# Kernel optimization log

Hardware: AMD Instinct MI355X
Metric: run time of the kernel (lower is better)

Reference implementation:

```python
import jax, jax.numpy as jnp
import numpy as np

B, N, D = 2, 2048, 1024
H = 16
HD = D // H  # head_dim = 64
EPS = 1e-5


def _layernorm(x, gamma, beta):
    mu = jnp.mean(x, axis=-1, keepdims=True)
    var = jnp.var(x, axis=-1, keepdims=True)
    return (x - mu) * jax.lax.rsqrt(var + EPS) * gamma + beta


def setup_inputs() -> dict:
    key = jax.random.key(0)
    ks = jax.random.split(key, 13)
    s = 1.0 / np.sqrt(D)
    return {
        "query": jax.random.normal(ks[0], (B, N, D), dtype=jnp.float32),
        "Wq": jax.random.uniform(ks[1], (D, D), jnp.float32, -s, s),
        "bq": jax.random.uniform(ks[2], (D,), jnp.float32, -s, s),
        "Wk": jax.random.uniform(ks[3], (D, D), jnp.float32, -s, s),
        "bk": jax.random.uniform(ks[4], (D,), jnp.float32, -s, s),
        "Wv": jax.random.uniform(ks[5], (D, D), jnp.float32, -s, s),
        "bv": jax.random.uniform(ks[6], (D,), jnp.float32, -s, s),
        "Wp": jax.random.uniform(ks[7], (D, D), jnp.float32, -s, s),
        "bp": jax.random.uniform(ks[8], (D,), jnp.float32, -s, s),
        "q_gamma": jnp.ones((HD,), jnp.float32),
        "q_beta": jnp.zeros((HD,), jnp.float32),
        "k_gamma": jnp.ones((HD,), jnp.float32),
        "k_beta": jnp.zeros((HD,), jnp.float32),
    }


def reference(query, Wq, bq, Wk, bk, Wv, bv, Wp, bp, q_gamma, q_beta, k_gamma, k_beta):
    # Linear projections (torch Linear: x @ W.T + b)
    def split_heads(x):  # [B,N,D] -> [B,H,N,HD]
        return x.reshape(B, N, H, HD).transpose(0, 2, 1, 3)

    Q = split_heads(query @ Wq.T + bq)
    K = split_heads(query @ Wk.T + bk)
    V = split_heads(query @ Wv.T + bv)

    # per-head QK LayerNorm
    Q = _layernorm(Q, q_gamma, q_beta)
    K = _layernorm(K, k_gamma, k_beta)

    scale = 1.0 / np.sqrt(HD)
    attn = jax.nn.softmax(jnp.einsum('bhqd,bhkd->bhqk', Q, K) * scale, axis=-1)
    # dropout_prob = 0.0 -> identity
    out = jnp.einsum('bhqk,bhkd->bqhd', attn, V).reshape(B, N, D)
    return out @ Wp.T + bp
```

## Files before the change

### kernel.cpp

```cpp
#include <hip/hip_runtime.h>
#include <math.h>

#define Bb 2
#define Nn 2048
#define Dd 1024
#define Hh 16
#define HD 64

typedef __attribute__((ext_vector_type(8))) short short8;
typedef __attribute__((ext_vector_type(4))) short short4v;
typedef __attribute__((ext_vector_type(4))) float floatx4;

__device__ __forceinline__ short f2bf(float x) {
    unsigned u = __float_as_uint(x);
    u += 0x7fffu + ((u >> 16) & 1u);
    return (short)(u >> 16);
}

#if defined(__has_builtin)
#  if __has_builtin(__builtin_amdgcn_mfma_f32_16x16x16bf16_1k)
#    define MFMA16(a, b, c) __builtin_amdgcn_mfma_f32_16x16x16bf16_1k(a, b, c, 0, 0, 0)
#  endif
#endif
#ifndef MFMA16
static __device__ __forceinline__ floatx4 mfma16_asm(short4v a, short4v b, floatx4 c) {
    asm volatile("v_mfma_f32_16x16x16_bf16 %0, %1, %2, %0" : "+v"(c) : "v"(a), "v"(b));
    return c;
}
#  define MFMA16(a, b, c) mfma16_asm(a, b, c)
#endif

__device__ __forceinline__ void gload16(const void* g, void* l) {
    __builtin_amdgcn_global_load_lds(
        (const __attribute__((address_space(1))) unsigned int*)g,
        (__attribute__((address_space(3))) unsigned int*)l,
        16, 0, 0);
}

#define QSCALE 0.18033688011112042f

__global__ __launch_bounds__(256) void cast_all(
    const float* __restrict__ x,
    const float* __restrict__ Wq, const float* __restrict__ Wk,
    const float* __restrict__ Wv, const float* __restrict__ Wp,
    short* __restrict__ xh, short* __restrict__ Wqh, short* __restrict__ Wkh,
    short* __restrict__ Wvh, short* __restrict__ Wph)
{
    const float* src; short* dst; int n4;
    switch (blockIdx.y) {
        case 0:  src = x;  dst = xh;  n4 = (Bb * Nn * Dd) / 4; break;
        case 1:  src = Wq; dst = Wqh; n4 = (Dd * Dd) / 4; break;
        case 2:  src = Wk; dst = Wkh; n4 = (Dd * Dd) / 4; break;
        case 3:  src = Wv; dst = Wvh; n4 = (Dd * Dd) / 4; break;
        default: src = Wp; dst = Wph; n4 = (Dd * Dd) / 4; break;
    }
    const int i = blockIdx.x * 256 + threadIdx.x;
    if (i >= n4) return;
    float4 v = ((const float4*)src)[i];
    short4v o;
    o.x = f2bf(v.x); o.y = f2bf(v.y); o.z = f2bf(v.z); o.w = f2bf(v.w);
    ((short4v*)dst)[i] = o;
}

__global__ __launch_bounds__(256) void qkv_ln_gemm(
    const short* __restrict__ xh,
    const short* __restrict__ Wqh, const short* __restrict__ Wkh,
    const short* __restrict__ Wvh,
    const float* __restrict__ bq, const float* __restrict__ bk,
    const float* __restrict__ bv,
    const float* __restrict__ qg, const float* __restrict__ qb,
    const float* __restrict__ kg, const float* __restrict__ kb,
    short* __restrict__ Qh, short* __restrict__ Kh, short* __restrict__ Vt)
{
    const int z = blockIdx.z;
    const short* A; const short* W;
    int rowBase, colBase, Nc;
    if (z < 2) { A = xh;  W = z ? Wkh : Wqh;
                 rowBase = blockIdx.x * 128; colBase = blockIdx.y * 128; Nc = Dd; }
    else       { A = Wvh; W = xh;
                 rowBase = blockIdx.y * 128; colBase = blockIdx.x * 128; Nc = Bb * Nn; }

    __shared__ __align__(16) short As[128 * 32];
    __shared__ __align__(16) short Ws[128 * 32];

    const int t    = threadIdx.x;
    const int w    = t >> 6;
    const int lane = t & 63;
    const int quad = lane >> 4;
    const int l15  = lane & 15;
    const int wy   = w >> 1;
    const int wx   = w & 1;

    const int r0 = t >> 2;
    const int kg4 = (t & 3) * 8;
    const short* aP = A + (size_t)(rowBase + r0) * Dd + kg4;
    const short* wP = W + (size_t)(colBase + r0) * Dd + kg4;
    const size_t rowskip = (size_t)64 * Dd;

    floatx4 acc[4][4];
    #pragma unroll
    for (int mi = 0; mi < 4; ++mi)
        #pragma unroll
        for (int ni = 0; ni < 4; ++ni)
            acc[mi][ni] = (floatx4){0.f, 0.f, 0.f, 0.f};

    for (int k0 = 0; k0 < Dd; k0 += 32) {
        gload16(aP,           &As[t * 8]);
        gload16(aP + rowskip, &As[(t + 256) * 8]);
        gload16(wP,           &Ws[t * 8]);
        gload16(wP + rowskip, &Ws[(t + 256) * 8]);
        aP += 32; wP += 32;
        __syncthreads();

        short8 af[4], bfr[4];
        #pragma unroll
        for (int i = 0; i < 4; ++i) {
            af[i]  = *(const short8*)&As[(wy * 64 + i * 16 + l15) * 32 + quad * 8];
            bfr[i] = *(const short8*)&Ws[(wx * 64 + i * 16 + l15) * 32 + quad * 8];
        }
        #pragma unroll
        for (int mi = 0; mi < 4; ++mi)
            #pragma unroll
            for (int ni = 0; ni < 4; ++ni)
                acc[mi][ni] = __builtin_amdgcn_mfma_f32_16x16x32_bf16(
                    af[mi], bfr[ni], acc[mi][ni], 0, 0, 0);
        __syncthreads();
    }

    if (z == 2) {
        #pragma unroll
        for (int mi = 0; mi < 4; ++mi) {
            #pragma unroll
            for (int r = 0; r < 4; ++r) {
                const size_t row = rowBase + wy * 64 + mi * 16 + quad * 4 + r;
                const float brv = bv[row];
                #pragma unroll
                for (int ni = 0; ni < 4; ++ni) {
                    const int col = colBase + wx * 64 + ni * 16 + l15;
                    Vt[row * (size_t)Nc + col] = f2bf(acc[mi][ni][r] + brv);
                }
            }
        }
    } else {
        const float* bias = z ? bk : bq;
        const float* gam  = z ? kg : qg;
        const float* bet  = z ? kb : qb;
        const float oscale = z ? 1.0f : QSCALE;
        short* out = z ? Kh : Qh;
        float bcol[4], g4[4], be4[4];
        #pragma unroll
        for (int ni = 0; ni < 4; ++ni) {
            const int ch = ni * 16 + l15;
            bcol[ni] = bias[colBase + wx * 64 + ch];
            g4[ni]   = gam[ch];
            be4[ni]  = bet[ch];
        }
        #pragma unroll
        for (int mi = 0; mi < 4; ++mi) {
            #pragma unroll
            for (int r = 0; r < 4; ++r) {
                const size_t row = rowBase + wy * 64 + mi * 16 + quad * 4 + r;
                float v[4], s = 0.f, s2 = 0.f;
                #pragma unroll
                for (int ni = 0; ni < 4; ++ni) {
                    v[ni] = acc[mi][ni][r] + bcol[ni];
                    s += v[ni]; s2 += v[ni] * v[ni];
                }
                #pragma unroll
                for (int d = 1; d < 16; d <<= 1) {
                    s  += __shfl_xor(s,  d, 16);
                    s2 += __shfl_xor(s2, d, 16);
                }
                const float mean = s * (1.0f / 64.0f);
                const float var  = s2 * (1.0f / 64.0f) - mean * mean;
                const float rr   = rsqrtf(var + 1e-5f);
                #pragma unroll
                for (int ni = 0; ni < 4; ++ni) {
                    const int col = colBase + wx * 64 + ni * 16 + l15;
                    out[row * (size_t)Dd + col] =
                        f2bf(((v[ni] - mean) * rr * g4[ni] + be4[ni]) * oscale);
                }
            }
        }
    }
}

__global__ __launch_bounds__(256) void gemm_mfma(
    const short* __restrict__ A, const short* __restrict__ W,
    const float* __restrict__ bias, float* __restrict__ Cf,
    int M, int K, int Nc)
{
    __shared__ __align__(16) short As[128 * 32];
    __shared__ __align__(16) short Ws[128 * 32];

    const int t    = threadIdx.x;
    const int w    = t >> 6;
    const int lane = t & 63;
    const int quad = lane >> 4;
    const int l15  = lane & 15;
    const int wy   = w >> 1;
    const int wx   = w & 1;
    const int rowBase = blockIdx.y * 128;
    const int colBase = blockIdx.x * 128;

    const int r0 = t >> 2;
    const int kg4 = (t & 3) * 8;
    const short* aP = A + (size_t)(rowBase + r0) * K + kg4;
    const short* wP = W + (size_t)(colBase + r0) * K + kg4;
    const size_t rowskip = (size_t)64 * K;

    floatx4 acc[4][4];
    #pragma unroll
    for (int mi = 0; mi < 4; ++mi)
        #pragma unroll
        for (int ni = 0; ni < 4; ++ni)
            acc[mi][ni] = (floatx4){0.f, 0.f, 0.f, 0.f};

    for (int k0 = 0; k0 < K; k0 += 32) {
        gload16(aP,           &As[t * 8]);
        gload16(aP + rowskip, &As[(t + 256) * 8]);
        gload16(wP,           &Ws[t * 8]);
        gload16(wP + rowskip, &Ws[(t + 256) * 8]);
        aP += 32; wP += 32;
        __syncthreads();

        short8 af[4], bfr[4];
        #pragma unroll
        for (int i = 0; i < 4; ++i) {
            af[i]  = *(const short8*)&As[(wy * 64 + i * 16 + l15) * 32 + quad * 8];
            bfr[i] = *(const short8*)&Ws[(wx * 64 + i * 16 + l15) * 32 + quad * 8];
        }
        #pragma unroll
        for (int mi = 0; mi < 4; ++mi)
            #pragma unroll
            for (int ni = 0; ni < 4; ++ni)
                acc[mi][ni] = __builtin_amdgcn_mfma_f32_16x16x32_bf16(
                    af[mi], bfr[ni], acc[mi][ni], 0, 0, 0);
        __syncthreads();
    }

    #pragma unroll
    for (int mi = 0; mi < 4; ++mi) {
        #pragma unroll
        for (int r = 0; r < 4; ++r) {
            const size_t row = rowBase + wy * 64 + mi * 16 + quad * 4 + r;
            #pragma unroll
            for (int ni = 0; ni < 4; ++ni) {
                const int col = colBase + wx * 64 + ni * 16 + l15;
                Cf[row * Nc + col] = acc[mi][ni][r] + bias[col];
            }
        }
    }
}

__global__ __launch_bounds__(256, 2) void flash_mfma(
    const short* __restrict__ Qh, const short* __restrict__ Kh,
    const short* __restrict__ Vt, short* __restrict__ ctx)
{
    const int qt = blockIdx.x;
    const int h  = blockIdx.y;
    const int b  = blockIdx.z;

    const int t    = threadIdx.x;
    const int w    = t >> 6;
    const int lane = t & 63;
    const int quad = lane >> 4;
    const int l15  = lane & 15;

    __shared__ __align__(16) short Ksh[64][72];
    __shared__ __align__(16) short Vsh[64][72];

    const size_t bhead = (size_t)b * Nn * Dd + (size_t)h * HD;

    short8 qf[2][2];
    #pragma unroll
    for (int qs = 0; qs < 2; ++qs) {
        const short* qp = Qh + bhead
            + (size_t)(qt * 128 + w * 32 + qs * 16 + l15) * Dd + quad * 8;
        qf[qs][0] = *(const short8*)qp;
        qf[qs][1] = *(const short8*)(qp + 32);
    }

    floatx4 accO[2][4], accL[2];
    #pragma unroll
    for (int qs = 0; qs < 2; ++qs) {
        #pragma unroll
        for (int n = 0; n < 4; ++n) accO[qs][n] = (floatx4){0.f, 0.f, 0.f, 0.f};
        accL[qs] = (floatx4){0.f, 0.f, 0.f, 0.f};
    }
    short4v ones;
    ones[0] = ones[1] = ones[2] = ones[3] = (short)0x3F80;

    const int s3  = t >> 3;
    const int c3  = ((t & 7) + (s3 & 7)) & 7;
    const int skg = c3 * 8;
    const short* kP = Kh + bhead + (size_t)s3 * Dd + skg;
    const short* vP = Vt + (size_t)(h * 64 + s3) * (Bb * Nn) + (size_t)b * Nn + skg;

    short8 kr0 = *(const short8*)kP;
    short8 kr1 = *(const short8*)(kP + 32 * Dd);
    short8 vr0 = *(const short8*)vP;
    short8 vr1 = *(const short8*)(vP + 32 * (Bb * Nn));

    for (int k0 = 0; k0 < Nn; k0 += 64) {
        *(short8*)&Ksh[s3][skg]      = kr0;
        *(short8*)&Ksh[s3 + 32][skg] = kr1;
        *(short8*)&Vsh[s3][skg]      = vr0;
        *(short8*)&Vsh[s3 + 32][skg] = vr1;
        __syncthreads();

        kP += 64 * Dd; vP += 64;
        kr0 = *(const short8*)kP;
        kr1 = *(const short8*)(kP + 32 * Dd);
        vr0 = *(const short8*)vP;
        vr1 = *(const short8*)(vP + 32 * (Bb * Nn));

        floatx4 accS[2][4];
        #pragma unroll
        for (int n = 0; n < 4; ++n) {
            short8 kf0 = *(const short8*)&Ksh[n * 16 + l15][quad * 8];
            short8 kf1 = *(const short8*)&Ksh[n * 16 + l15][32 + quad * 8];
            #pragma unroll
            for (int qs = 0; qs < 2; ++qs) {
                floatx4 zz = (floatx4){0.f, 0.f, 0.f, 0.f};
                zz = __builtin_amdgcn_mfma_f32_16x16x32_bf16(kf0, qf[qs][0], zz, 0, 0, 0);
                zz = __builtin_amdgcn_mfma_f32_16x16x32_bf16(kf1, qf[qs][1], zz, 0, 0, 0);
                accS[qs][n] = zz;
            }
        }

        short4v pfrag[2][4];
        #pragma unroll
        for (int qs = 0; qs < 2; ++qs) {
            #pragma unroll
            for (int n = 0; n < 4; ++n) {
                const unsigned u0 = __float_as_uint(exp2f(accS[qs][n][0]));
                const unsigned u1 = __float_as_uint(exp2f(accS[qs][n][1]));
                const unsigned u2 = __float_as_uint(exp2f(accS[qs][n][2]));
                const unsigned u3 = __float_as_uint(exp2f(accS[qs][n][3]));
                union { uint2 u; short4v s; } pk;
                pk.u.x = __builtin_amdgcn_perm(u1, u0, 0x07060302u);
                pk.u.y = __builtin_amdgcn_perm(u3, u2, 0x07060302u);
                pfrag[qs][n] = pk.s;
                accL[qs] = MFMA16(pk.s, ones, accL[qs]);
            }
        }

        #pragma unroll
        for (int n = 0; n < 4; ++n) {
            #pragma unroll
            for (int c = 0; c < 4; ++c) {
                const short4v vb =
                    *(const short4v*)&Vsh[c * 16 + l15][n * 16 + quad * 4];
                accO[0][c] = MFMA16(pfrag[0][n], vb, accO[0][c]);
                accO[1][c] = MFMA16(pfrag[1][n], vb, accO[1][c]);
            }
        }
        __syncthreads();
    }

    #pragma unroll
    for (int qs = 0; qs < 2; ++qs) {
        #pragma unroll
        for (int r = 0; r < 4; ++r) {
            const float lr = 1.0f / accL[qs][r];
            short* dst = ctx + (size_t)((b * Nn) + qt * 128 + w * 32 + qs * 16
                                        + quad * 4 + r) * Dd + h * HD + l15;
            #pragma unroll
            for (int n = 0; n < 4; ++n) dst[n * 16] = f2bf(accO[qs][n][r] * lr);
        }
    }
}

extern "C" void kernel_launch(void* const* d_in, const int* in_sizes, int n_in,
                              void* d_out, int out_size, void* d_ws, size_t ws_size,
                              hipStream_t stream) {
    const float* x   = (const float*)d_in[0];
    const float* Wq  = (const float*)d_in[1];
    const float* bq  = (const float*)d_in[2];
    const float* Wk  = (const float*)d_in[3];
    const float* bk  = (const float*)d_in[4];
    const float* Wv  = (const float*)d_in[5];
    const float* bv  = (const float*)d_in[6];
    const float* Wp  = (const float*)d_in[7];
    const float* bp  = (const float*)d_in[8];
    const float* qg  = (const float*)d_in[9];
    const float* qb  = (const float*)d_in[10];
    const float* kg  = (const float*)d_in[11];
    const float* kb  = (const float*)d_in[12];
    float* out = (float*)d_out;

    const size_t S = (size_t)Bb * Nn * Dd;
    short* wsb = (short*)d_ws;
    short* xh   = wsb;
    short* Vt   = wsb + S;
    short* Kh   = wsb + 2 * S;
    short* Qh   = wsb + 3 * S;
    short* ctxh = wsb + 4 * S;
    short* Wqh  = wsb + 5 * S;
    short* Wkh  = Wqh + Dd * Dd;
    short* Wvh  = Wkh + Dd * Dd;
    short* Wph  = Wvh + Dd * Dd;

    const int M = Bb * Nn;

    cast_all<<<dim3(4096, 5), 256, 0, stream>>>(x, Wq, Wk, Wv, Wp,
                                                xh, Wqh, Wkh, Wvh, Wph);

    qkv_ln_gemm<<<dim3(M / 128, Dd / 128, 3), 256, 0, stream>>>(
        xh, Wqh, Wkh, Wvh, bq, bk, bv, qg, qb, kg, kb, Qh, Kh, Vt);

    flash_mfma<<<dim3(Nn / 128, Hh, Bb), 256, 0, stream>>>(Qh, Kh, Vt, ctxh);

    gemm_mfma<<<dim3(Dd / 128, M / 128, 1), 256, 0, stream>>>(
        ctxh, Wph, bp, out, M, Dd, Dd);
}
```

Measured before the change: 239.0 us.

## Split flash attention work across 8 waves with 16 query rows each

Result: faster. 231.2 us (-3.3%).

```diff
diff --git a/kernel.cpp b/kernel.cpp
--- a/kernel.cpp
+++ b/kernel.cpp
@@ -253,7 +253,7 @@
     }
 }
 
-__global__ __launch_bounds__(256, 2) void flash_mfma(
+__global__ __launch_bounds__(512, 4) void flash_mfma(
     const short* __restrict__ Qh, const short* __restrict__ Kh,
     const short* __restrict__ Vt, short* __restrict__ ctx)
 {
@@ -268,26 +268,22 @@
     const int l15  = lane & 15;
 
     __shared__ __align__(16) short Ksh[64][72];
-    __shared__ __align__(16) short Vsh[64][72];
+    __shared__ __align__(16) short Vsh[64][76];
 
     const size_t bhead = (size_t)b * Nn * Dd + (size_t)h * HD;
 
-    short8 qf[2][2];
+    short8 qf[2];
+    {
+        const short* qp = Qh + bhead
+            + (size_t)(qt * 128 + w * 16 + l15) * Dd + quad * 8;
+        qf[0] = *(const short8*)qp;
+        qf[1] = *(const short8*)(qp + 32);
+    }
+
+    floatx4 accO[4], accL;
     #pragma unroll
-    for (int qs = 0; qs < 2; ++qs) {
-        const short* qp = Qh + bhead
-            + (size_t)(qt * 128 + w * 32 + qs * 16 + l15) * Dd + quad * 8;
-        qf[qs][0] = *(const short8*)qp;
-        qf[qs][1] = *(const short8*)(qp + 32);
-    }
-
-    floatx4 accO[2][4], accL[2];
-    #pragma unroll
-    for (int qs = 0; qs < 2; ++qs) {
-        #pragma unroll
-        for (int n = 0; n < 4; ++n) accO[qs][n] = (floatx4){0.f, 0.f, 0.f, 0.f};
-        accL[qs] = (floatx4){0.f, 0.f, 0.f, 0.f};
-    }
+    for (int n = 0; n < 4; ++n) accO[n] = (floatx4){0.f, 0.f, 0.f, 0.f};
+    accL = (floatx4){0.f, 0.f, 0.f, 0.f};
     short4v ones;
     ones[0] = ones[1] = ones[2] = ones[3] = (short)0x3F80;
 
@@ -297,53 +293,45 @@
     const short* kP = Kh + bhead + (size_t)s3 * Dd + skg;
     const short* vP = Vt + (size_t)(h * 64 + s3) * (Bb * Nn) + (size_t)b * Nn + skg;
 
-    short8 kr0 = *(const short8*)kP;
-    short8 kr1 = *(const short8*)(kP + 32 * Dd);
-    short8 vr0 = *(const short8*)vP;
-    short8 vr1 = *(const short8*)(vP + 32 * (Bb * Nn));
+    short8 kr = *(const short8*)kP;
+    short8 vr = *(const short8*)vP;
 
     for (int k0 = 0; k0 < Nn; k0 += 64) {
-        *(short8*)&Ksh[s3][skg]      = kr0;
-        *(short8*)&Ksh[s3 + 32][skg] = kr1;
-        *(short8*)&Vsh[s3][skg]      = vr0;
-        *(short8*)&Vsh[s3 + 32][skg] = vr1;
+        *(short8*)&Ksh[s3][skg] = kr;
+        {
+            union { short8 v8; short4v v4[2]; } vv; vv.v8 = vr;
+            *(short4v*)&Vsh[s3][skg]     = vv.v4[0];
+            *(short4v*)&Vsh[s3][skg + 4] = vv.v4[1];
+        }
         __syncthreads();
 
         kP += 64 * Dd; vP += 64;
-        kr0 = *(const short8*)kP;
-        kr1 = *(const short8*)(kP + 32 * Dd);
-        vr0 = *(const short8*)vP;
-        vr1 = *(const short8*)(vP + 32 * (Bb * Nn));
-
-        floatx4 accS[2][4];
+        kr = *(const short8*)kP;
+        vr = *(const short8*)vP;
+
+        floatx4 accS[4];
         #pragma unroll
         for (int n = 0; n < 4; ++n) {
             short8 kf0 = *(const short8*)&Ksh[n * 16 + l15][quad * 8];
             short8 kf1 = *(const short8*)&Ksh[n * 16 + l15][32 + quad * 8];
-            #pragma unroll
-            for (int qs = 0; qs < 2; ++qs) {
-                floatx4 zz = (floatx4){0.f, 0.f, 0.f, 0.f};
-                zz = __builtin_amdgcn_mfma_f32_16x16x32_bf16(kf0, qf[qs][0], zz, 0, 0, 0);
-                zz = __builtin_amdgcn_mfma_f32_16x16x32_bf16(kf1, qf[qs][1], zz, 0, 0, 0);
-                accS[qs][n] = zz;
-            }
-        }
-
-        short4v pfrag[2][4];
-        #pragma unroll
-        for (int qs = 0; qs < 2; ++qs) {
-            #pragma unroll
-            for (int n = 0; n < 4; ++n) {
-                const unsigned u0 = __float_as_uint(exp2f(accS[qs][n][0]));
-                const unsigned u1 = __float_as_uint(exp2f(accS[qs][n][1]));
-                const unsigned u2 = __float_as_uint(exp2f(accS[qs][n][2]));
-                const unsigned u3 = __float_as_uint(exp2f(accS[qs][n][3]));
-                union { uint2 u; short4v s; } pk;
-                pk.u.x = __builtin_amdgcn_perm(u1, u0, 0x07060302u);
-                pk.u.y = __builtin_amdgcn_perm(u3, u2, 0x07060302u);
-                pfrag[qs][n] = pk.s;
-                accL[qs] = MFMA16(pk.s, ones, accL[qs]);
-            }
+            floatx4 zz = (floatx4){0.f, 0.f, 0.f, 0.f};
+            zz = __builtin_amdgcn_mfma_f32_16x16x32_bf16(kf0, qf[0], zz, 0, 0, 0);
+            zz = __builtin_amdgcn_mfma_f32_16x16x32_bf16(kf1, qf[1], zz, 0, 0, 0);
+            accS[n] = zz;
+        }
+
+        short4v pfrag[4];
+        #pragma unroll
+        for (int n = 0; n < 4; ++n) {
+            const unsigned u0 = __float_as_uint(exp2f(accS[n][0]));
+            const unsigned u1 = __float_as_uint(exp2f(accS[n][1]));
+            const unsigned u2 = __float_as_uint(exp2f(accS[n][2]));
+            const unsigned u3 = __float_as_uint(exp2f(accS[n][3]));
+            union { uint2 u; short4v s; } pk;
+            pk.u.x = __builtin_amdgcn_perm(u1, u0, 0x07060302u);
+            pk.u.y = __builtin_amdgcn_perm(u3, u2, 0x07060302u);
+            pfrag[n] = pk.s;
+            accL = MFMA16(pk.s, ones, accL);
         }
 
         #pragma unroll
@@ -352,23 +340,19 @@
             for (int c = 0; c < 4; ++c) {
                 const short4v vb =
                     *(const short4v*)&Vsh[c * 16 + l15][n * 16 + quad * 4];
-                accO[0][c] = MFMA16(pfrag[0][n], vb, accO[0][c]);
-                accO[1][c] = MFMA16(pfrag[1][n], vb, accO[1][c]);
+                accO[c] = MFMA16(pfrag[n], vb, accO[c]);
             }
         }
         __syncthreads();
     }
 
     #pragma unroll
-    for (int qs = 0; qs < 2; ++qs) {
-        #pragma unroll
-        for (int r = 0; r < 4; ++r) {
-            const float lr = 1.0f / accL[qs][r];
-            short* dst = ctx + (size_t)((b * Nn) + qt * 128 + w * 32 + qs * 16
-                                        + quad * 4 + r) * Dd + h * HD + l15;
-            #pragma unroll
-            for (int n = 0; n < 4; ++n) dst[n * 16] = f2bf(accO[qs][n][r] * lr);
-        }
+    for (int r = 0; r < 4; ++r) {
+        const float lr = 1.0f / accL[r];
+        short* dst = ctx + (size_t)((b * Nn) + qt * 128 + w * 16
+                                    + quad * 4 + r) * Dd + h * HD + l15;
+        #pragma unroll
+        for (int n = 0; n < 4; ++n) dst[n * 16] = f2bf(accO[n][r] * lr);
     }
 }
 
@@ -410,7 +394,7 @@
     qkv_ln_gemm<<<dim3(M / 128, Dd / 128, 3), 256, 0, stream>>>(
         xh, Wqh, Wkh, Wvh, bq, bk, bv, qg, qb, kg, kb, Qh, Kh, Vt);
 
-    flash_mfma<<<dim3(Nn / 128, Hh, Bb), 256, 0, stream>>>(Qh, Kh, Vt, ctxh);
+    flash_mfma<<<dim3(Nn / 128, Hh, Bb), 512, 0, stream>>>(Qh, Kh, Vt, ctxh);
 
     gemm_mfma<<<dim3(Dd / 128, M / 128, 1), 256, 0, stream>>>(
         ctxh, Wph, bp, out, M, Dd, Dd);
```
